# Kernel optimization log

Hardware: AMD Instinct MI355X
Metric: run time of the kernel (lower is better)

## Reference

```python
import jax, jax.numpy as jnp
import numpy as np

DIM = 768
NUM_HEADS = 12
HEAD_DIM = DIM // NUM_HEADS  # 64
H = W = 48


def setup_inputs() -> dict:
    key = jax.random.key(0)
    ks = jax.random.split(key, 7)
    x = jax.random.normal(ks[0], (2, H, W, DIM), dtype=jnp.float32)
    # qkv Linear: stored as [in, out] for x @ W convention
    qkv_w = jax.random.normal(ks[1], (DIM, 3 * DIM), dtype=jnp.float32) * (DIM ** -0.5)
    qkv_b = jax.random.normal(ks[2], (3 * DIM,), dtype=jnp.float32) * 0.02
    proj_w = jax.random.normal(ks[3], (DIM, DIM), dtype=jnp.float32) * (DIM ** -0.5)
    proj_b = jax.random.normal(ks[4], (DIM,), dtype=jnp.float32) * 0.02
    # decomposed relative position tables (trunc_normal std=0.02 ~ normal*0.02)
    rel_pos_h = jax.random.normal(ks[5], (2 * H - 1, HEAD_DIM), dtype=jnp.float32) * 0.02
    rel_pos_w = jax.random.normal(ks[6], (2 * W - 1, HEAD_DIM), dtype=jnp.float32) * 0.02
    return {"x": x, "qkv_w": qkv_w, "qkv_b": qkv_b, "proj_w": proj_w,
            "proj_b": proj_b, "rel_pos_h": rel_pos_h, "rel_pos_w": rel_pos_w}


def _get_rel_pos(size, rel_pos):
    # q_size == k_size == size; table already has 2*size-1 entries, no interp
    coords = jnp.arange(size)[:, None] - jnp.arange(size)[None, :] + (size - 1)
    return rel_pos[coords]  # [size, size, head_dim]


def reference(x, qkv_w, qkv_b, proj_w, proj_b, rel_pos_h, rel_pos_w):
    B, h, w, dim = x.shape
    nh, hd = NUM_HEADS, HEAD_DIM
    S = h * w
    scale = hd ** -0.5
    qkv = (x.reshape(B, S, dim) @ qkv_w + qkv_b).reshape(B, S, 3, nh, hd)
    qkv = jnp.transpose(qkv, (2, 0, 3, 1, 4)).reshape(3, B * nh, S, hd)
    q, k, v = qkv[0], qkv[1], qkv[2]
    attn = jnp.einsum("bqc,bkc->bqk", q * scale, k)  # [B*nh, S, S]
    # decomposed relative position bias
    Rh = _get_rel_pos(h, rel_pos_h)  # [h, h, hd]
    Rw = _get_rel_pos(w, rel_pos_w)  # [w, w, hd]
    r_q = q.reshape(B * nh, h, w, hd)
    rel_h = jnp.einsum("bhwc,hkc->bhwk", r_q, Rh)  # [B*nh, h, w, h]
    rel_w = jnp.einsum("bhwc,wkc->bhwk", r_q, Rw)  # [B*nh, h, w, w]
    attn = (attn.reshape(B * nh, h, w, h, w)
            + rel_h[:, :, :, :, None]
            + rel_w[:, :, :, None, :]).reshape(B * nh, S, S)
    attn = jax.nn.softmax(attn, axis=-1)
    out = (attn @ v).reshape(B, nh, h, w, hd)
    out = jnp.transpose(out, (0, 2, 3, 1, 4)).reshape(B, h, w, dim)
    return out @ proj_w + proj_b
```

## Files before the change

### kernel.cpp

```cpp
#include <hip/hip_runtime.h>
#include <hip/hip_fp16.h>

#define HD 64
#define SEQ 2304

typedef unsigned short u16;
typedef unsigned int u32;
using f32x4 = __attribute__((ext_vector_type(4))) float;
using s16x8 = __attribute__((ext_vector_type(8))) short;

static __device__ __forceinline__ u16 f2bf(float x) {
  union { float f; u32 u; } a; a.f = x;
  u32 r = a.u + 0x7fffu + ((a.u >> 16) & 1u);
  return (u16)(r >> 16);
}
static __device__ __forceinline__ float bf2f(u16 h) {
  union { float f; u32 u; } a; a.u = ((u32)h) << 16; return a.f;
}

__global__ __launch_bounds__(256) void conv_wT_k(
    const float* __restrict__ src, u16* __restrict__ dhi, u16* __restrict__ dlo,
    int K, int N)
{
  __shared__ u32 t[64][65];
  const int tid = threadIdx.x;
  const int n0 = blockIdx.x * 64, k0 = blockIdx.y * 64;
  const int r = tid >> 2, c0 = (tid & 3) * 16;
  const float* sp = src + (size_t)(k0 + r) * N + n0 + c0;
#pragma unroll
  for (int j = 0; j < 16; j += 4) {
    f32x4 v = *(const f32x4*)(sp + j);
#pragma unroll
    for (int e = 0; e < 4; e++) {
      float x = v[e];
      u16 h = f2bf(x);
      u16 l = f2bf(x - bf2f(h));
      t[r][c0 + j + e] = (u32)h | ((u32)l << 16);
    }
  }
  __syncthreads();
  u16 hb[16], lb[16];
#pragma unroll
  for (int j = 0; j < 16; j++) {
    u32 p = t[c0 + j][r];
    hb[j] = (u16)(p & 0xffffu);
    lb[j] = (u16)(p >> 16);
  }
  size_t off = (size_t)(n0 + r) * K + k0 + c0;
  *(uint4*)(dhi + off)     = *(uint4*)&hb[0];
  *(uint4*)(dhi + off + 8) = *(uint4*)&hb[8];
  *(uint4*)(dlo + off)     = *(uint4*)&lb[0];
  *(uint4*)(dlo + off + 8) = *(uint4*)&lb[8];
}

__global__ __launch_bounds__(256) void qkv_mfma_k(
    const float* __restrict__ x, const u16* __restrict__ bthi, const u16* __restrict__ btlo,
    const float* __restrict__ bias,
    float* __restrict__ qbuf, u16* __restrict__ khi, u16* __restrict__ klo,
    u16* __restrict__ vhi, u16* __restrict__ vlo)
{
  __shared__ __align__(16) u16 Ah[128*40], Al[128*40], Bh2[128*40], Bl2[128*40];
  const int tid = threadIdx.x;
  const int lane = tid & 63, wid = tid >> 6;
  const int g = lane >> 4, ql = lane & 15;
  const int wr = wid >> 1, wc = wid & 1;
  const int c0 = blockIdx.x * 128, r0 = blockIdx.y * 128;
  const int srow = tid >> 1, half = tid & 1;

  const float* ag = x + (size_t)(r0 + srow) * 768 + half * 16;
  const u16* bgh = bthi + (size_t)(c0 + srow) * 768 + half * 16;
  const u16* bgl = btlo + (size_t)(c0 + srow) * 768 + half * 16;

  f32x4 pa[4]; uint4 pbh[2], pbl[2];
#pragma unroll
  for (int j = 0; j < 4; j++) pa[j] = *(const f32x4*)(ag + j * 4);
  pbh[0] = *(const uint4*)bgh; pbh[1] = *(const uint4*)(bgh + 8);
  pbl[0] = *(const uint4*)bgl; pbl[1] = *(const uint4*)(bgl + 8);

  f32x4 acc[4][4] = {};

  for (int ks = 0; ks < 24; ks++) {
    __syncthreads();
    {
      u16 hb[16], lb[16];
#pragma unroll
      for (int j = 0; j < 16; j++) {
        float xv = pa[j >> 2][j & 3];
        u16 h = f2bf(xv);
        hb[j] = h; lb[j] = f2bf(xv - bf2f(h));
      }
      u16* d1 = Ah + srow * 40 + half * 16;
      u16* d2 = Al + srow * 40 + half * 16;
      *(uint4*)d1 = *(uint4*)&hb[0];
      *(uint4*)(d1 + 8) = *(uint4*)&hb[8];
      *(uint4*)d2 = *(uint4*)&lb[0];
      *(uint4*)(d2 + 8) = *(uint4*)&lb[8];
      u16* d3 = Bh2 + srow * 40 + half * 16;
      u16* d4 = Bl2 + srow * 40 + half * 16;
      *(uint4*)d3 = pbh[0]; *(uint4*)(d3 + 8) = pbh[1];
      *(uint4*)d4 = pbl[0]; *(uint4*)(d4 + 8) = pbl[1];
    }
    __syncthreads();
    if (ks < 23) {
      const float* a2 = ag + (ks + 1) * 32;
#pragma unroll
      for (int j = 0; j < 4; j++) pa[j] = *(const f32x4*)(a2 + j * 4);
      pbh[0] = *(const uint4*)(bgh + (ks + 1) * 32);
      pbh[1] = *(const uint4*)(bgh + (ks + 1) * 32 + 8);
      pbl[0] = *(const uint4*)(bgl + (ks + 1) * 32);
      pbl[1] = *(const uint4*)(bgl + (ks + 1) * 32 + 8);
    }
    s16x8 bfh[4], bfl[4];
#pragma unroll
    for (int nt = 0; nt < 4; nt++) {
      bfh[nt] = *(const s16x8*)(Bh2 + (wc * 64 + nt * 16 + ql) * 40 + g * 8);
      bfl[nt] = *(const s16x8*)(Bl2 + (wc * 64 + nt * 16 + ql) * 40 + g * 8);
    }
#pragma unroll
    for (int mt = 0; mt < 4; mt++) {
      s16x8 ah = *(const s16x8*)(Ah + (wr * 64 + mt * 16 + ql) * 40 + g * 8);
      s16x8 al = *(const s16x8*)(Al + (wr * 64 + mt * 16 + ql) * 40 + g * 8);
#pragma unroll
      for (int nt = 0; nt < 4; nt++) {
        acc[mt][nt] = __builtin_amdgcn_mfma_f32_16x16x32_bf16(ah, bfh[nt], acc[mt][nt], 0, 0, 0);
        acc[mt][nt] = __builtin_amdgcn_mfma_f32_16x16x32_bf16(ah, bfl[nt], acc[mt][nt], 0, 0, 0);
        acc[mt][nt] = __builtin_amdgcn_mfma_f32_16x16x32_bf16(al, bfh[nt], acc[mt][nt], 0, 0, 0);
      }
    }
  }
  const int col0 = c0 + wc * 64;
  const int row0 = r0 + wr * 64;
  const int hb36 = col0 >> 6;
  const int which = hb36 / 12, head = hb36 - (hb36 / 12) * 12;
  const int b = row0 / 2304;
  const int sb = row0 - b * 2304;
  const int bh = b * 12 + head;
  float bb[4];
#pragma unroll
  for (int nt = 0; nt < 4; nt++) bb[nt] = bias[col0 + nt * 16 + ql];
  if (which == 0) {
#pragma unroll
    for (int mt = 0; mt < 4; mt++)
#pragma unroll
      for (int nt = 0; nt < 4; nt++)
#pragma unroll
        for (int r = 0; r < 4; r++) {
          int s = sb + mt * 16 + g * 4 + r;
          qbuf[((size_t)bh * SEQ + s) * 64 + nt * 16 + ql] = acc[mt][nt][r] + bb[nt];
        }
  } else {
    const int kt = sb >> 6;
    const size_t tile = ((size_t)bh * 36 + kt) * 4096;
    if (which == 1) {
#pragma unroll
      for (int mt = 0; mt < 4; mt++)
#pragma unroll
        for (int nt = 0; nt < 4; nt++) {
          int pc = (nt >> 1) * 32 + (ql >> 2) * 8 + (nt & 1) * 4 + (ql & 3);
#pragma unroll
          for (int r = 0; r < 4; r++) {
            int key = mt * 16 + g * 4 + r;
            float xv = acc[mt][nt][r] + bb[nt];
            u16 h = f2bf(xv);
            khi[tile + key * 64 + pc] = h;
            klo[tile + key * 64 + pc] = f2bf(xv - bf2f(h));
          }
        }
    } else {
#pragma unroll
      for (int mt = 0; mt < 4; mt++)
#pragma unroll
        for (int nt = 0; nt < 4; nt++)
#pragma unroll
          for (int r = 0; r < 4; r++) {
            int d = nt * 16 + ql;
            int vc = (mt >> 1) * 32 + g * 8 + (mt & 1) * 4 + r;
            float xv = acc[mt][nt][r] + bb[nt];
            u16 h = f2bf(xv);
            vhi[tile + d * 64 + vc] = h;
            vlo[tile + d * 64 + vc] = f2bf(xv - bf2f(h));
          }
    }
  }
}

__global__ __launch_bounds__(512) void attn_k(
    const float* __restrict__ qb,
    const u16* __restrict__ khi, const u16* __restrict__ klo,
    const u16* __restrict__ vhi, const u16* __restrict__ vlo,
    const float* __restrict__ rph, const float* __restrict__ rpw,
    float* __restrict__ ao)
{
  __shared__ __align__(16) char pool[49664];
  u16* KhiL = (u16*)pool;
  u16* KloL = (u16*)(pool + 9216);
  u16* VhL  = (u16*)(pool + 18432);
  u16* VlL  = (u16*)(pool + 27648);
  __half* Bh = (__half*)(pool + 36864);
  __half* Bw = (__half*)(pool + 43008);
  float* m_s = (float*)(pool + 49152);
  float* l_s = (float*)(pool + 49408);
  float* qlds = (float*)pool;
  float* o_s  = (float*)pool;

  const int tid  = threadIdx.x;
  const int lane = tid & 63;
  const int wid  = tid >> 6;
  const int g    = lane >> 4;
  const int ql   = lane & 15;
  const int wq   = wid & 3;
  const int hh   = wid >> 2;
  const int qt   = blockIdx.x;
  const int bh   = blockIdx.y;
  const int s0   = qt * 64;

  {
    int row = tid >> 3, c0 = (tid & 7) * 8;
    const float* src = qb + ((size_t)bh * SEQ + s0 + row) * HD + c0;
    f32x4 v0 = *(const f32x4*)src;
    f32x4 v1 = *(const f32x4*)(src + 4);
    *(f32x4*)&qlds[row * 68 + c0]     = v0;
    *(f32x4*)&qlds[row * 68 + c0 + 4] = v1;
  }
  __syncthreads();

  s16x8 qfh[2], qfl[2];
  {
    int qrow = wq * 16 + ql;
#pragma unroll
    for (int ds = 0; ds < 2; ds++) {
#pragma unroll
      for (int h2 = 0; h2 < 2; h2++) {
        f32x4 qv = *(const f32x4*)&qlds[qrow * 68 + g * 4 + h2 * 16 + ds * 32];
#pragma unroll
        for (int j = 0; j < 4; j++) {
          float xx = qv[j];
          u16 hi = f2bf(xx);
          u16 lo = f2bf(xx - bf2f(hi));
          qfh[ds][h2 * 4 + j] = (short)hi;
          qfl[ds][h2 * 4 + j] = (short)lo;
        }
      }
    }
  }

  const size_t tbK = (size_t)bh * 36 * 4096;
  const int srow = tid >> 3;
  const int sch  = ((tid & 7) - (srow & 7)) & 7;
  const size_t soff = (size_t)srow * 64 + sch * 8;
  uint4 rkh = *(const uint4*)(khi + tbK + soff);
  uint4 rkl = *(const uint4*)(klo + tbK + soff);
  uint4 rvh = *(const uint4*)(vhi + tbK + soff);
  uint4 rvl = *(const uint4*)(vlo + tbK + soff);

  for (int i = tid; i < 64 * 96; i += 512) {
    int q = i / 96, j = i - (i / 96) * 96;
    int s = s0 + q;
    int qhg = s / 48, qw = s - qhg * 48;
    const float* tab;
    int ridx, col;
    if (j < 48) { col = j;      ridx = qhg - j + 47;        tab = rph; }
    else        { col = j - 48; ridx = qw - (j - 48) + 47;  tab = rpw; }
    const float* rp = tab + (size_t)ridx * HD;
    const float* qp = &qlds[q * 68];
    float s1 = 0.f;
#pragma unroll 4
    for (int d = 0; d < 64; d += 4) {
      f32x4 a = *(const f32x4*)(qp + d);
      f32x4 bv = *(const f32x4*)(rp + d);
      s1 += a[0]*bv[0] + a[1]*bv[1] + a[2]*bv[2] + a[3]*bv[3];
    }
    if (j < 48) Bh[col * 64 + q] = __float2half_rn(s1);
    else        Bw[col * 64 + q] = __float2half_rn(s1);
  }

  float m_r = -3.0e38f, l_r = 0.f;
  f32x4 oacc[4] = {};
  const int q64b = wq * 16 + ql;

  for (int kt = 0; kt < 36; kt++) {
    __syncthreads();
    *(uint4*)(KhiL + srow * 72 + sch * 8) = rkh;
    *(uint4*)(KloL + srow * 72 + sch * 8) = rkl;
    *(uint4*)(VhL  + srow * 72 + sch * 8) = rvh;
    *(uint4*)(VlL  + srow * 72 + sch * 8) = rvl;
    __syncthreads();
    if (kt < 35) {
      size_t tb = tbK + (size_t)(kt + 1) * 4096;
      rkh = *(const uint4*)(khi + tb + soff);
      rkl = *(const uint4*)(klo + tb + soff);
      rvh = *(const uint4*)(vhi + tb + soff);
      rvl = *(const uint4*)(vlo + tb + soff);
    }

    f32x4 sacc[2] = {};
#pragma unroll
    for (int ds = 0; ds < 2; ds++) {
#pragma unroll
      for (int t2 = 0; t2 < 2; t2++) {
        int row = (hh * 2 + t2) * 16 + ql;
        s16x8 af = *(const s16x8*)(KhiL + row * 72 + ds * 32 + g * 8);
        s16x8 al = *(const s16x8*)(KloL + row * 72 + ds * 32 + g * 8);
        sacc[t2] = __builtin_amdgcn_mfma_f32_16x16x32_bf16(af, qfh[ds], sacc[t2], 0, 0, 0);
        sacc[t2] = __builtin_amdgcn_mfma_f32_16x16x32_bf16(af, qfl[ds], sacc[t2], 0, 0, 0);
        sacc[t2] = __builtin_amdgcn_mfma_f32_16x16x32_bf16(al, qfh[ds], sacc[t2], 0, 0, 0);
      }
    }

    float lg[8];
    float tmax = -3.0e38f;
#pragma unroll
    for (int t2 = 0; t2 < 2; t2++)
#pragma unroll
      for (int r = 0; r < 4; r++) {
        u32 kg = (u32)(kt * 64 + hh * 32 + t2 * 16 + g * 4 + r);
        u32 kh = kg / 48u;
        u32 kw = kg - kh * 48u;
        float x = sacc[t2][r] * 0.125f
                + __half2float(Bh[(int)kh * 64 + q64b])
                + __half2float(Bw[(int)kw * 64 + q64b]);
        lg[t2 * 4 + r] = x;
        tmax = fmaxf(tmax, x);
      }
    tmax = fmaxf(tmax, __shfl_xor(tmax, 16));
    tmax = fmaxf(tmax, __shfl_xor(tmax, 32));
    if (__any(tmax > m_r + 6.0f)) {
      float mnew = fmaxf(m_r, tmax);
      float corr = __expf(m_r - mnew);
      l_r *= corr;
      m_r = mnew;
      float cq[4];
#pragma unroll
      for (int r = 0; r < 4; r++) cq[r] = __shfl(corr, g * 4 + r);
#pragma unroll
      for (int dt = 0; dt < 4; dt++)
#pragma unroll
        for (int r = 0; r < 4; r++) oacc[dt][r] *= cq[r];
    }
    float psum = 0.f;
    s16x8 pfh, pfl;
#pragma unroll
    for (int j = 0; j < 8; j++) {
      float p = __expf(lg[j] - m_r);
      psum += p;
      u16 hi = f2bf(p);
      pfh[j] = (short)hi;
      pfl[j] = (short)f2bf(p - bf2f(hi));
    }
    psum += __shfl_xor(psum, 16);
    psum += __shfl_xor(psum, 32);
    l_r += psum;

#pragma unroll
    for (int dt = 0; dt < 4; dt++) {
      int row = ql + 16 * dt;
      s16x8 bhf = *(const s16x8*)(VhL + row * 72 + hh * 32 + g * 8);
      s16x8 blf = *(const s16x8*)(VlL + row * 72 + hh * 32 + g * 8);
      oacc[dt] = __builtin_amdgcn_mfma_f32_16x16x32_bf16(pfh, bhf, oacc[dt], 0, 0, 0);
      oacc[dt] = __builtin_amdgcn_mfma_f32_16x16x32_bf16(pfh, blf, oacc[dt], 0, 0, 0);
      oacc[dt] = __builtin_amdgcn_mfma_f32_16x16x32_bf16(pfl, bhf, oacc[dt], 0, 0, 0);
    }
  }

  __syncthreads();
  if (hh == 1) {
    if (g == 0) { m_s[wq * 16 + ql] = m_r; l_s[wq * 16 + ql] = l_r; }
#pragma unroll
    for (int dt = 0; dt < 4; dt++)
#pragma unroll
      for (int r = 0; r < 4; r++)
        o_s[(wq * 16 + g * 4 + r) * 68 + ql + 16 * dt] = oacc[dt][r];
  }
  __syncthreads();
  if (hh == 0) {
    float m2 = m_s[wq * 16 + ql];
    float l2 = l_s[wq * 16 + ql];
    float mf = fmaxf(m_r, m2);
    float c1 = __expf(m_r - mf);
    float c2 = __expf(m2 - mf);
    float lf = l_r * c1 + l2 * c2;
    float c1q[4], c2q[4], lfq[4];
#pragma unroll
    for (int r = 0; r < 4; r++) {
      c1q[r] = __shfl(c1, g * 4 + r);
      c2q[r] = __shfl(c2, g * 4 + r);
      lfq[r] = __shfl(lf, g * 4 + r);
    }
    const int b = bh / 12, head = bh - (bh / 12) * 12;
#pragma unroll
    for (int dt = 0; dt < 4; dt++)
#pragma unroll
      for (int r = 0; r < 4; r++) {
        float oo = oacc[dt][r] * c1q[r]
                 + o_s[(wq * 16 + g * 4 + r) * 68 + ql + 16 * dt] * c2q[r];
        int s = s0 + wq * 16 + g * 4 + r;
        ao[((size_t)b * SEQ + s) * 768 + head * 64 + ql + 16 * dt] = oo / lfq[r];
      }
  }
}

__global__ __launch_bounds__(256) void proj_mfma_k(
    const float* __restrict__ a, const u16* __restrict__ bthi, const u16* __restrict__ btlo,
    const float* __restrict__ bias, float* __restrict__ out)
{
  __shared__ __align__(16) u16 Ah[128*40], Al[128*40], Bh2[128*40], Bl2[128*40];
  const int tid = threadIdx.x;
  const int lane = tid & 63, wid = tid >> 6;
  const int g = lane >> 4, ql = lane & 15;
  const int wr = wid >> 1, wc = wid & 1;
  const int c0 = blockIdx.x * 128, r0 = blockIdx.y * 128;
  const int srow = tid >> 1, half = tid & 1;

  const float* ag = a + (size_t)(r0 + srow) * 768 + half * 16;
  const u16* bgh = bthi + (size_t)(c0 + srow) * 768 + half * 16;
  const u16* bgl = btlo + (size_t)(c0 + srow) * 768 + half * 16;

  f32x4 pa[4]; uint4 pbh[2], pbl[2];
#pragma unroll
  for (int j = 0; j < 4; j++) pa[j] = *(const f32x4*)(ag + j * 4);
  pbh[0] = *(const uint4*)bgh; pbh[1] = *(const uint4*)(bgh + 8);
  pbl[0] = *(const uint4*)bgl; pbl[1] = *(const uint4*)(bgl + 8);

  f32x4 acc[4][4] = {};

  for (int ks = 0; ks < 24; ks++) {
    __syncthreads();
    {
      u16 hb[16], lb[16];
#pragma unroll
      for (int j = 0; j < 16; j++) {
        float xv = pa[j >> 2][j & 3];
        u16 h = f2bf(xv);
        hb[j] = h; lb[j] = f2bf(xv - bf2f(h));
      }
      u16* d1 = Ah + srow * 40 + half * 16;
      u16* d2 = Al + srow * 40 + half * 16;
      *(uint4*)d1 = *(uint4*)&hb[0];
      *(uint4*)(d1 + 8) = *(uint4*)&hb[8];
      *(uint4*)d2 = *(uint4*)&lb[0];
      *(uint4*)(d2 + 8) = *(uint4*)&lb[8];
      u16* d3 = Bh2 + srow * 40 + half * 16;
      u16* d4 = Bl2 + srow * 40 + half * 16;
      *(uint4*)d3 = pbh[0]; *(uint4*)(d3 + 8) = pbh[1];
      *(uint4*)d4 = pbl[0]; *(uint4*)(d4 + 8) = pbl[1];
    }
    __syncthreads();
    if (ks < 23) {
      const float* a2 = ag + (ks + 1) * 32;
#pragma unroll
      for (int j = 0; j < 4; j++) pa[j] = *(const f32x4*)(a2 + j * 4);
      pbh[0] = *(const uint4*)(bgh + (ks + 1) * 32);
      pbh[1] = *(const uint4*)(bgh + (ks + 1) * 32 + 8);
      pbl[0] = *(const uint4*)(bgl + (ks + 1) * 32);
      pbl[1] = *(const uint4*)(bgl + (ks + 1) * 32 + 8);
    }
    s16x8 bfh[4], bfl[4];
#pragma unroll
    for (int nt = 0; nt < 4; nt++) {
      bfh[nt] = *(const s16x8*)(Bh2 + (wc * 64 + nt * 16 + ql) * 40 + g * 8);
      bfl[nt] = *(const s16x8*)(Bl2 + (wc * 64 + nt * 16 + ql) * 40 + g * 8);
    }
#pragma unroll
    for (int mt = 0; mt < 4; mt++) {
      s16x8 ah = *(const s16x8*)(Ah + (wr * 64 + mt * 16 + ql) * 40 + g * 8);
      s16x8 al = *(const s16x8*)(Al + (wr * 64 + mt * 16 + ql) * 40 + g * 8);
#pragma unroll
      for (int nt = 0; nt < 4; nt++) {
        acc[mt][nt] = __builtin_amdgcn_mfma_f32_16x16x32_bf16(ah, bfh[nt], acc[mt][nt], 0, 0, 0);
        acc[mt][nt] = __builtin_amdgcn_mfma_f32_16x16x32_bf16(ah, bfl[nt], acc[mt][nt], 0, 0, 0);
        acc[mt][nt] = __builtin_amdgcn_mfma_f32_16x16x32_bf16(al, bfh[nt], acc[mt][nt], 0, 0, 0);
      }
    }
  }
  const int col0 = c0 + wc * 64;
  const int row0 = r0 + wr * 64;
  float bb[4];
#pragma unroll
  for (int nt = 0; nt < 4; nt++) bb[nt] = bias[col0 + nt * 16 + ql];
#pragma unroll
  for (int mt = 0; mt < 4; mt++)
#pragma unroll
    for (int nt = 0; nt < 4; nt++)
#pragma unroll
      for (int r = 0; r < 4; r++)
        out[(size_t)(row0 + mt * 16 + g * 4 + r) * 768 + col0 + nt * 16 + ql] =
            acc[mt][nt][r] + bb[nt];
}

extern "C" void kernel_launch(void* const* d_in, const int* in_sizes, int n_in,
                              void* d_out, int out_size, void* d_ws, size_t ws_size,
                              hipStream_t stream) {
  const float* x      = (const float*)d_in[0];
  const float* qkv_w  = (const float*)d_in[1];
  const float* qkv_b  = (const float*)d_in[2];
  const float* proj_w = (const float*)d_in[3];
  const float* proj_b = (const float*)d_in[4];
  const float* rph    = (const float*)d_in[5];
  const float* rpw    = (const float*)d_in[6];
  float* out = (float*)d_out;
  float* ws  = (float*)d_ws;

  const size_t SZ = (size_t)24 * SEQ * HD;
  float* qbuf = ws;
  u16* khi = (u16*)(ws + SZ);
  u16* klo = khi + SZ;
  u16* vhi = klo + SZ;
  u16* vlo = vhi + SZ;
  float* ao = ws + 3 * SZ;
  u16* wqThi = (u16*)(ws + 4 * SZ);
  u16* wqTlo = wqThi + 768 * 2304;
  u16* wpThi = wqTlo + 768 * 2304;
  u16* wpTlo = wpThi + 768 * 768;

  conv_wT_k <<<dim3(36, 12), 256, 0, stream>>>(qkv_w, wqThi, wqTlo, 768, 2304);
  conv_wT_k <<<dim3(12, 12), 256, 0, stream>>>(proj_w, wpThi, wpTlo, 768, 768);
  qkv_mfma_k<<<dim3(18, 36), 256, 0, stream>>>(x, wqThi, wqTlo, qkv_b,
                                               qbuf, khi, klo, vhi, vlo);
  attn_k    <<<dim3(36, 24), 512, 0, stream>>>(qbuf, khi, klo, vhi, vlo, rph, rpw, ao);
  proj_mfma_k<<<dim3(6, 36), 256, 0, stream>>>(ao, wpThi, wpTlo, proj_b, out);
}
```

Baseline: 522.1 us.

## Presplit activations, truncate bf16 split, pad bias LDS, reorder attention grid

Adds a pre-pass that splits x into bf16 hi/lo arrays, so the QKV GEMM loads ready-made halves instead of converting in its main loop. The attention kernel now writes packed hi/lo output that the projection GEMM unpacks without converting. Rounding-based bf16 conversion is replaced with truncation for the hi part. Attention also pads the bias tables in LDS (row stride 66), hoists the row-bias lookup out of the inner loop, raises wave priority around MFMA blocks, and swaps the grid order so the head index comes first. These changes trade an extra kernel launch and more workspace traffic for less conversion ALU work and fewer LDS bank conflicts.

Result: slower. 587.8 us (+12.6%).

```diff
diff --git a/kernel.cpp b/kernel.cpp
--- a/kernel.cpp
+++ b/kernel.cpp
@@ -9,13 +9,30 @@
 using f32x4 = __attribute__((ext_vector_type(4))) float;
 using s16x8 = __attribute__((ext_vector_type(8))) short;
 
-static __device__ __forceinline__ u16 f2bf(float x) {
-  union { float f; u32 u; } a; a.f = x;
-  u32 r = a.u + 0x7fffu + ((a.u >> 16) & 1u);
-  return (u16)(r >> 16);
-}
 static __device__ __forceinline__ float bf2f(u16 h) {
   union { float f; u32 u; } a; a.u = ((u32)h) << 16; return a.f;
+}
+static __device__ __forceinline__ void split2(float x, u16& h, u16& l) {
+  u32 u = __float_as_uint(x);
+  h = (u16)(u >> 16);
+  float r = x - __uint_as_float(u & 0xffff0000u);
+  l = (u16)(__float_as_uint(r) >> 16);
+}
+
+__global__ __launch_bounds__(256) void conv_split_k(
+    const float* __restrict__ src, u16* __restrict__ dhi, u16* __restrict__ dlo)
+{
+  const size_t i = ((size_t)blockIdx.x * 256 + threadIdx.x) * 8;
+  f32x4 a = *(const f32x4*)(src + i);
+  f32x4 b = *(const f32x4*)(src + i + 4);
+  u16 h[8], l[8];
+#pragma unroll
+  for (int j = 0; j < 8; j++) {
+    float x = j < 4 ? a[j] : b[j - 4];
+    split2(x, h[j], l[j]);
+  }
+  *(uint4*)(dhi + i) = *(uint4*)&h[0];
+  *(uint4*)(dlo + i) = *(uint4*)&l[0];
 }
 
 __global__ __launch_bounds__(256) void conv_wT_k(
@@ -32,9 +49,8 @@
     f32x4 v = *(const f32x4*)(sp + j);
 #pragma unroll
     for (int e = 0; e < 4; e++) {
-      float x = v[e];
-      u16 h = f2bf(x);
-      u16 l = f2bf(x - bf2f(h));
+      u16 h, l;
+      split2(v[e], h, l);
       t[r][c0 + j + e] = (u32)h | ((u32)l << 16);
     }
   }
@@ -54,7 +70,8 @@
 }
 
 __global__ __launch_bounds__(256) void qkv_mfma_k(
-    const float* __restrict__ x, const u16* __restrict__ bthi, const u16* __restrict__ btlo,
+    const u16* __restrict__ xhi, const u16* __restrict__ xlo,
+    const u16* __restrict__ bthi, const u16* __restrict__ btlo,
     const float* __restrict__ bias,
     float* __restrict__ qbuf, u16* __restrict__ khi, u16* __restrict__ klo,
     u16* __restrict__ vhi, u16* __restrict__ vlo)
@@ -67,13 +84,14 @@
   const int c0 = blockIdx.x * 128, r0 = blockIdx.y * 128;
   const int srow = tid >> 1, half = tid & 1;
 
-  const float* ag = x + (size_t)(r0 + srow) * 768 + half * 16;
+  const u16* agh = xhi + (size_t)(r0 + srow) * 768 + half * 16;
+  const u16* agl = xlo + (size_t)(r0 + srow) * 768 + half * 16;
   const u16* bgh = bthi + (size_t)(c0 + srow) * 768 + half * 16;
   const u16* bgl = btlo + (size_t)(c0 + srow) * 768 + half * 16;
 
-  f32x4 pa[4]; uint4 pbh[2], pbl[2];
-#pragma unroll
-  for (int j = 0; j < 4; j++) pa[j] = *(const f32x4*)(ag + j * 4);
+  uint4 pah[2], pal[2], pbh[2], pbl[2];
+  pah[0] = *(const uint4*)agh; pah[1] = *(const uint4*)(agh + 8);
+  pal[0] = *(const uint4*)agl; pal[1] = *(const uint4*)(agl + 8);
   pbh[0] = *(const uint4*)bgh; pbh[1] = *(const uint4*)(bgh + 8);
   pbl[0] = *(const uint4*)bgl; pbl[1] = *(const uint4*)(bgl + 8);
 
@@ -82,33 +100,22 @@
   for (int ks = 0; ks < 24; ks++) {
     __syncthreads();
     {
-      u16 hb[16], lb[16];
-#pragma unroll
-      for (int j = 0; j < 16; j++) {
-        float xv = pa[j >> 2][j & 3];
-        u16 h = f2bf(xv);
-        hb[j] = h; lb[j] = f2bf(xv - bf2f(h));
-      }
       u16* d1 = Ah + srow * 40 + half * 16;
       u16* d2 = Al + srow * 40 + half * 16;
-      *(uint4*)d1 = *(uint4*)&hb[0];
-      *(uint4*)(d1 + 8) = *(uint4*)&hb[8];
-      *(uint4*)d2 = *(uint4*)&lb[0];
-      *(uint4*)(d2 + 8) = *(uint4*)&lb[8];
       u16* d3 = Bh2 + srow * 40 + half * 16;
       u16* d4 = Bl2 + srow * 40 + half * 16;
+      *(uint4*)d1 = pah[0]; *(uint4*)(d1 + 8) = pah[1];
+      *(uint4*)d2 = pal[0]; *(uint4*)(d2 + 8) = pal[1];
       *(uint4*)d3 = pbh[0]; *(uint4*)(d3 + 8) = pbh[1];
       *(uint4*)d4 = pbl[0]; *(uint4*)(d4 + 8) = pbl[1];
     }
     __syncthreads();
     if (ks < 23) {
-      const float* a2 = ag + (ks + 1) * 32;
-#pragma unroll
-      for (int j = 0; j < 4; j++) pa[j] = *(const f32x4*)(a2 + j * 4);
-      pbh[0] = *(const uint4*)(bgh + (ks + 1) * 32);
-      pbh[1] = *(const uint4*)(bgh + (ks + 1) * 32 + 8);
-      pbl[0] = *(const uint4*)(bgl + (ks + 1) * 32);
-      pbl[1] = *(const uint4*)(bgl + (ks + 1) * 32 + 8);
+      const int o = (ks + 1) * 32;
+      pah[0] = *(const uint4*)(agh + o); pah[1] = *(const uint4*)(agh + o + 8);
+      pal[0] = *(const uint4*)(agl + o); pal[1] = *(const uint4*)(agl + o + 8);
+      pbh[0] = *(const uint4*)(bgh + o); pbh[1] = *(const uint4*)(bgh + o + 8);
+      pbl[0] = *(const uint4*)(bgl + o); pbl[1] = *(const uint4*)(bgl + o + 8);
     }
     s16x8 bfh[4], bfl[4];
 #pragma unroll
@@ -160,10 +167,10 @@
 #pragma unroll
           for (int r = 0; r < 4; r++) {
             int key = mt * 16 + g * 4 + r;
-            float xv = acc[mt][nt][r] + bb[nt];
-            u16 h = f2bf(xv);
+            u16 h, l;
+            split2(acc[mt][nt][r] + bb[nt], h, l);
             khi[tile + key * 64 + pc] = h;
-            klo[tile + key * 64 + pc] = f2bf(xv - bf2f(h));
+            klo[tile + key * 64 + pc] = l;
           }
         }
     } else {
@@ -175,31 +182,35 @@
           for (int r = 0; r < 4; r++) {
             int d = nt * 16 + ql;
             int vc = (mt >> 1) * 32 + g * 8 + (mt & 1) * 4 + r;
-            float xv = acc[mt][nt][r] + bb[nt];
-            u16 h = f2bf(xv);
+            u16 h, l;
+            split2(acc[mt][nt][r] + bb[nt], h, l);
             vhi[tile + d * 64 + vc] = h;
-            vlo[tile + d * 64 + vc] = f2bf(xv - bf2f(h));
+            vlo[tile + d * 64 + vc] = l;
           }
     }
   }
 }
 
+#define BH_OFF 36864
+#define BW_OFF (BH_OFF + 49*66*2)
+#define MS_OFF (BW_OFF + 48*66*2)
+#define LS_OFF (MS_OFF + 256)
 __global__ __launch_bounds__(512) void attn_k(
     const float* __restrict__ qb,
     const u16* __restrict__ khi, const u16* __restrict__ klo,
     const u16* __restrict__ vhi, const u16* __restrict__ vlo,
     const float* __restrict__ rph, const float* __restrict__ rpw,
-    float* __restrict__ ao)
+    u32* __restrict__ aop)
 {
-  __shared__ __align__(16) char pool[49664];
+  __shared__ __align__(16) char pool[LS_OFF + 256];
   u16* KhiL = (u16*)pool;
   u16* KloL = (u16*)(pool + 9216);
   u16* VhL  = (u16*)(pool + 18432);
   u16* VlL  = (u16*)(pool + 27648);
-  __half* Bh = (__half*)(pool + 36864);
-  __half* Bw = (__half*)(pool + 43008);
-  float* m_s = (float*)(pool + 49152);
-  float* l_s = (float*)(pool + 49408);
+  __half* Bh = (__half*)(pool + BH_OFF);
+  __half* Bw = (__half*)(pool + BW_OFF);
+  float* m_s = (float*)(pool + MS_OFF);
+  float* l_s = (float*)(pool + LS_OFF);
   float* qlds = (float*)pool;
   float* o_s  = (float*)pool;
 
@@ -210,8 +221,8 @@
   const int ql   = lane & 15;
   const int wq   = wid & 3;
   const int hh   = wid >> 2;
-  const int qt   = blockIdx.x;
-  const int bh   = blockIdx.y;
+  const int bh   = blockIdx.x;
+  const int qt   = blockIdx.y;
   const int s0   = qt * 64;
 
   {
@@ -234,9 +245,8 @@
         f32x4 qv = *(const f32x4*)&qlds[qrow * 68 + g * 4 + h2 * 16 + ds * 32];
 #pragma unroll
         for (int j = 0; j < 4; j++) {
-          float xx = qv[j];
-          u16 hi = f2bf(xx);
-          u16 lo = f2bf(xx - bf2f(hi));
+          u16 hi, lo;
+          split2(qv[j], hi, lo);
           qfh[ds][h2 * 4 + j] = (short)hi;
           qfl[ds][h2 * 4 + j] = (short)lo;
         }
@@ -270,8 +280,8 @@
       f32x4 bv = *(const f32x4*)(rp + d);
       s1 += a[0]*bv[0] + a[1]*bv[1] + a[2]*bv[2] + a[3]*bv[3];
     }
-    if (j < 48) Bh[col * 64 + q] = __float2half_rn(s1);
-    else        Bw[col * 64 + q] = __float2half_rn(s1);
+    if (j < 48) Bh[col * 66 + q] = __float2half_rn(s1);
+    else        Bw[col * 66 + q] = __float2half_rn(s1);
   }
 
   float m_r = -3.0e38f, l_r = 0.f;
@@ -294,6 +304,7 @@
     }
 
     f32x4 sacc[2] = {};
+    __builtin_amdgcn_s_setprio(1);
 #pragma unroll
     for (int ds = 0; ds < 2; ds++) {
 #pragma unroll
@@ -306,20 +317,25 @@
         sacc[t2] = __builtin_amdgcn_mfma_f32_16x16x32_bf16(al, qfh[ds], sacc[t2], 0, 0, 0);
       }
     }
-
+    __builtin_amdgcn_s_setprio(0);
+
+    u32 kg0 = (u32)(kt * 64 + hh * 32);
+    u32 kh0 = kg0 / 48u;
+    int kw0 = (int)(kg0 - kh0 * 48u);
+    float bh0 = __half2float(Bh[kh0 * 66 + q64b]);
+    float bh1 = __half2float(Bh[(kh0 + 1) * 66 + q64b]);
     float lg[8];
     float tmax = -3.0e38f;
 #pragma unroll
     for (int t2 = 0; t2 < 2; t2++)
 #pragma unroll
       for (int r = 0; r < 4; r++) {
-        u32 kg = (u32)(kt * 64 + hh * 32 + t2 * 16 + g * 4 + r);
-        u32 kh = kg / 48u;
-        u32 kw = kg - kh * 48u;
-        float x = sacc[t2][r] * 0.125f
-                + __half2float(Bh[(int)kh * 64 + q64b])
-                + __half2float(Bw[(int)kw * 64 + q64b]);
-        lg[t2 * 4 + r] = x;
+        int j = t2 * 4 + r;
+        int w = kw0 + t2 * 16 + g * 4 + r;
+        bool wrap = w >= 48;
+        float bw = __half2float(Bw[(wrap ? w - 48 : w) * 66 + q64b]);
+        float x = sacc[t2][r] * 0.125f + (wrap ? bh1 : bh0) + bw;
+        lg[j] = x;
         tmax = fmaxf(tmax, x);
       }
     tmax = fmaxf(tmax, __shfl_xor(tmax, 16));
@@ -343,14 +359,16 @@
     for (int j = 0; j < 8; j++) {
       float p = __expf(lg[j] - m_r);
       psum += p;
-      u16 hi = f2bf(p);
+      u16 hi, lo;
+      split2(p, hi, lo);
       pfh[j] = (short)hi;
-      pfl[j] = (short)f2bf(p - bf2f(hi));
+      pfl[j] = (short)lo;
     }
     psum += __shfl_xor(psum, 16);
     psum += __shfl_xor(psum, 32);
     l_r += psum;
 
+    __builtin_amdgcn_s_setprio(1);
 #pragma unroll
     for (int dt = 0; dt < 4; dt++) {
       int row = ql + 16 * dt;
@@ -360,11 +378,12 @@
       oacc[dt] = __builtin_amdgcn_mfma_f32_16x16x32_bf16(pfh, blf, oacc[dt], 0, 0, 0);
       oacc[dt] = __builtin_amdgcn_mfma_f32_16x16x32_bf16(pfl, bhf, oacc[dt], 0, 0, 0);
     }
+    __builtin_amdgcn_s_setprio(0);
   }
 
   __syncthreads();
   if (hh == 1) {
-    if (g == 0) { m_s[wq * 16 + ql] = m_r; l_s[wq * 16 + ql] = l_r; }
+    if (g == 0) { m_s[q64b] = m_r; l_s[q64b] = l_r; }
 #pragma unroll
     for (int dt = 0; dt < 4; dt++)
 #pragma unroll
@@ -373,8 +392,8 @@
   }
   __syncthreads();
   if (hh == 0) {
-    float m2 = m_s[wq * 16 + ql];
-    float l2 = l_s[wq * 16 + ql];
+    float m2 = m_s[q64b];
+    float l2 = l_s[q64b];
     float mf = fmaxf(m_r, m2);
     float c1 = __expf(m_r - mf);
     float c2 = __expf(m2 - mf);
@@ -393,14 +412,19 @@
       for (int r = 0; r < 4; r++) {
         float oo = oacc[dt][r] * c1q[r]
                  + o_s[(wq * 16 + g * 4 + r) * 68 + ql + 16 * dt] * c2q[r];
+        float on = oo / lfq[r];
         int s = s0 + wq * 16 + g * 4 + r;
-        ao[((size_t)b * SEQ + s) * 768 + head * 64 + ql + 16 * dt] = oo / lfq[r];
+        size_t idx = ((size_t)b * SEQ + s) * 768 + head * 64 + ql + 16 * dt;
+        u16 h, l;
+        split2(on, h, l);
+        aop[idx] = (u32)h | ((u32)l << 16);
       }
   }
 }
 
 __global__ __launch_bounds__(256) void proj_mfma_k(
-    const float* __restrict__ a, const u16* __restrict__ bthi, const u16* __restrict__ btlo,
+    const u32* __restrict__ aop,
+    const u16* __restrict__ bthi, const u16* __restrict__ btlo,
     const float* __restrict__ bias, float* __restrict__ out)
 {
   __shared__ __align__(16) u16 Ah[128*40], Al[128*40], Bh2[128*40], Bl2[128*40];
@@ -411,13 +435,13 @@
   const int c0 = blockIdx.x * 128, r0 = blockIdx.y * 128;
   const int srow = tid >> 1, half = tid & 1;
 
-  const float* ag = a + (size_t)(r0 + srow) * 768 + half * 16;
+  const u32* ag = aop + (size_t)(r0 + srow) * 768 + half * 16;
   const u16* bgh = bthi + (size_t)(c0 + srow) * 768 + half * 16;
   const u16* bgl = btlo + (size_t)(c0 + srow) * 768 + half * 16;
 
-  f32x4 pa[4]; uint4 pbh[2], pbl[2];
-#pragma unroll
-  for (int j = 0; j < 4; j++) pa[j] = *(const f32x4*)(ag + j * 4);
+  uint4 paw[4]; uint4 pbh[2], pbl[2];
+#pragma unroll
+  for (int j = 0; j < 4; j++) paw[j] = *(const uint4*)(ag + j * 4);
   pbh[0] = *(const uint4*)bgh; pbh[1] = *(const uint4*)(bgh + 8);
   pbl[0] = *(const uint4*)bgl; pbl[1] = *(const uint4*)(bgl + 8);
 
@@ -427,32 +451,28 @@
     __syncthreads();
     {
       u16 hb[16], lb[16];
+      const u32* pw = (const u32*)&paw[0];
 #pragma unroll
       for (int j = 0; j < 16; j++) {
-        float xv = pa[j >> 2][j & 3];
-        u16 h = f2bf(xv);
-        hb[j] = h; lb[j] = f2bf(xv - bf2f(h));
+        hb[j] = (u16)(pw[j] & 0xffffu);
+        lb[j] = (u16)(pw[j] >> 16);
       }
       u16* d1 = Ah + srow * 40 + half * 16;
       u16* d2 = Al + srow * 40 + half * 16;
-      *(uint4*)d1 = *(uint4*)&hb[0];
-      *(uint4*)(d1 + 8) = *(uint4*)&hb[8];
-      *(uint4*)d2 = *(uint4*)&lb[0];
-      *(uint4*)(d2 + 8) = *(uint4*)&lb[8];
       u16* d3 = Bh2 + srow * 40 + half * 16;
       u16* d4 = Bl2 + srow * 40 + half * 16;
+      *(uint4*)d1 = *(uint4*)&hb[0]; *(uint4*)(d1 + 8) = *(uint4*)&hb[8];
+      *(uint4*)d2 = *(uint4*)&lb[0]; *(uint4*)(d2 + 8) = *(uint4*)&lb[8];
       *(uint4*)d3 = pbh[0]; *(uint4*)(d3 + 8) = pbh[1];
       *(uint4*)d4 = pbl[0]; *(uint4*)(d4 + 8) = pbl[1];
     }
     __syncthreads();
     if (ks < 23) {
-      const float* a2 = ag + (ks + 1) * 32;
-#pragma unroll
-      for (int j = 0; j < 4; j++) pa[j] = *(const f32x4*)(a2 + j * 4);
-      pbh[0] = *(const uint4*)(bgh + (ks + 1) * 32);
-      pbh[1] = *(const uint4*)(bgh + (ks + 1) * 32 + 8);
-      pbl[0] = *(const uint4*)(bgl + (ks + 1) * 32);
-      pbl[1] = *(const uint4*)(bgl + (ks + 1) * 32 + 8);
+      const int o = (ks + 1) * 32;
+#pragma unroll
+      for (int j = 0; j < 4; j++) paw[j] = *(const uint4*)(ag + o + j * 4);
+      pbh[0] = *(const uint4*)(bgh + o); pbh[1] = *(const uint4*)(bgh + o + 8);
+      pbl[0] = *(const uint4*)(bgl + o); pbl[1] = *(const uint4*)(bgl + o + 8);
     }
     s16x8 bfh[4], bfl[4];
 #pragma unroll
@@ -506,16 +526,19 @@
   u16* klo = khi + SZ;
   u16* vhi = klo + SZ;
   u16* vlo = vhi + SZ;
-  float* ao = ws + 3 * SZ;
-  u16* wqThi = (u16*)(ws + 4 * SZ);
+  u16* xhi = (u16*)(ws + 3 * SZ);
+  u16* xlo = xhi + SZ;
+  u32* aop = (u32*)(ws + 4 * SZ);
+  u16* wqThi = (u16*)(ws + 5 * SZ);
   u16* wqTlo = wqThi + 768 * 2304;
   u16* wpThi = wqTlo + 768 * 2304;
   u16* wpTlo = wpThi + 768 * 768;
 
+  conv_split_k<<<1728, 256, 0, stream>>>(x, xhi, xlo);
   conv_wT_k <<<dim3(36, 12), 256, 0, stream>>>(qkv_w, wqThi, wqTlo, 768, 2304);
   conv_wT_k <<<dim3(12, 12), 256, 0, stream>>>(proj_w, wpThi, wpTlo, 768, 768);
-  qkv_mfma_k<<<dim3(18, 36), 256, 0, stream>>>(x, wqThi, wqTlo, qkv_b,
+  qkv_mfma_k<<<dim3(18, 36), 256, 0, stream>>>(xhi, xlo, wqThi, wqTlo, qkv_b,
                                                qbuf, khi, klo, vhi, vlo);
-  attn_k    <<<dim3(36, 24), 512, 0, stream>>>(qbuf, khi, klo, vhi, vlo, rph, rpw, ao);
-  proj_mfma_k<<<dim3(6, 36), 256, 0, stream>>>(ao, wpThi, wpTlo, proj_b, out);
-}
+  attn_k    <<<dim3(24, 36), 512, 0, stream>>>(qbuf, khi, klo, vhi, vlo, rph, rpw, aop);
+  proj_mfma_k<<<dim3(6, 36), 256, 0, stream>>>(aop, wpThi, wpTlo, proj_b, out);
+}
```
